# Performance work log

Measured on AMD Instinct MI355X. Metric: run time of the kernel, lower is better.

Reference implementation:

```python
import jax, jax.numpy as jnp
import numpy as np
from math import sqrt

INPUT_SIZE = 1024
HIDDEN_SIZE = 1024
OUTPUT_SIZE = 512
BATCH = 64
SEQ = 512


def _uniform(key, shape, stdv):
    return jax.random.uniform(key, shape, jnp.float32, -stdv, stdv)


def setup_inputs() -> dict:
    key = jax.random.key(0)
    ks = jax.random.split(key, 20)
    stdv = 1.0 / sqrt(HIDDEN_SIZE)
    H, I, O = HIDDEN_SIZE, INPUT_SIZE, OUTPUT_SIZE
    inp = {
        "X": jax.random.normal(ks[0], (BATCH, SEQ, I), jnp.float32),
        "c0": jnp.zeros((H, 1), jnp.float32),
        "h0": jnp.zeros((H, 1), jnp.float32),
        "w_hi": _uniform(ks[1], (H, H), stdv), "w_xi": _uniform(ks[2], (H, I), stdv),
        "b_hi": _uniform(ks[3], (H, 1), stdv), "b_xi": _uniform(ks[4], (H, 1), stdv),
        "w_hf": _uniform(ks[5], (H, H), stdv), "w_xf": _uniform(ks[6], (H, I), stdv),
        "b_hf": _uniform(ks[7], (H, 1), stdv), "b_xf": _uniform(ks[8], (H, 1), stdv),
        "w_ho": _uniform(ks[9], (H, H), stdv), "w_xo": _uniform(ks[10], (H, I), stdv),
        "b_ho": _uniform(ks[11], (H, 1), stdv), "b_xo": _uniform(ks[12], (H, 1), stdv),
        "w_hg": _uniform(ks[13], (H, H), stdv), "w_xg": _uniform(ks[14], (H, I), stdv),
        "b_hg": _uniform(ks[15], (H, 1), stdv), "b_xg": _uniform(ks[16], (H, 1), stdv),
        "w": _uniform(ks[17], (O, H), stdv),
    }
    return inp


def reference(X, c0, h0,
              w_hi, w_xi, b_hi, b_xi,
              w_hf, w_xf, b_hf, b_xf,
              w_ho, w_xo, b_ho, b_xo,
              w_hg, w_xg, b_hg, b_xg, w):
    B = X.shape[0]
    # state kept as (B, H); biases squeezed to (H,)
    bi = (b_hi + b_xi)[:, 0]
    bf = (b_hf + b_xf)[:, 0]
    bo = (b_ho + b_xo)[:, 0]
    bg = (b_hg + b_xg)[:, 0]
    h0b = jnp.broadcast_to(h0[:, 0], (B, h0.shape[0]))
    c0b = jnp.broadcast_to(c0[:, 0], (B, c0.shape[0]))

    def step(carry, x_t):  # x_t: (B, I)
        h, c = carry
        i = jax.nn.sigmoid(h @ w_hi.T + x_t @ w_xi.T + bi)
        f = jax.nn.sigmoid(h @ w_hf.T + x_t @ w_xf.T + bf)
        o = jax.nn.sigmoid(h @ w_ho.T + x_t @ w_xo.T + bo)
        g = jnp.tanh(h @ w_hg.T + x_t @ w_xg.T + bg)
        c = f * c + i * g
        h = o * jnp.tanh(c)
        return (h, c), None

    (h, c), _ = jax.lax.scan(step, (h0b, c0b), jnp.swapaxes(X, 0, 1))
    out = h @ w.T  # (B, O)
    return out[:, :, None]  # match torch output shape (B, O, 1)
```

## Files before the change

### kernel.cpp

```cpp
#include <hip/hip_runtime.h>


typedef short short8 __attribute__((ext_vector_type(8)));
typedef float f32x4 __attribute__((ext_vector_type(4)));

typedef __attribute__((address_space(1))) const unsigned int glb_u32;
typedef __attribute__((address_space(3))) unsigned int lds_u32;

#define SEQL  512
#define POISON 0xFFFFFFFFFFFFFFFFull
#define BUFU64 16384

__device__ __forceinline__ unsigned short f2bf(float f) {
    unsigned int u = __builtin_bit_cast(unsigned int, f);
    u += 0x7FFFu + ((u >> 16) & 1u);
    return (unsigned short)(u >> 16);
}
__device__ __forceinline__ float bf2f(unsigned short s) {
    unsigned int u = ((unsigned int)s) << 16;
    return __builtin_bit_cast(float, u);
}
__device__ __forceinline__ float sigmoidf_fast(float x) {
    return 1.f / (1.f + __expf(-x));
}
__device__ __forceinline__ float tanhf_fast(float x) {
    return 1.f - 2.f / (1.f + __expf(2.f * x));
}
__device__ __forceinline__ void gld_lds16(const unsigned short* g, unsigned short* l) {
    __builtin_amdgcn_global_load_lds((glb_u32*)g, (lds_u32*)l, 16, 0, 0);
}

__global__ void k_pack_w(const float* __restrict__ w0, const float* __restrict__ w1,
                         const float* __restrict__ w2, const float* __restrict__ w3,
                         unsigned short* __restrict__ dst) {
    int idx4 = blockIdx.x * blockDim.x + threadIdx.x;
    int np = idx4 >> 8;
    int k4 = (idx4 & 255) * 4;
    int g = np & 3, r = np >> 2;
    const float* src = (g == 0) ? w0 : (g == 1) ? w1 : (g == 2) ? w2 : w3;
    float4 v = *(const float4*)(src + r * 1024 + k4);
    ushort4 o;
    o.x = f2bf(v.x); o.y = f2bf(v.y); o.z = f2bf(v.z); o.w = f2bf(v.w);
    *(ushort4*)(dst + (size_t)np * 1024 + k4) = o;
}

__global__ void k_misc(const float* __restrict__ b_hi, const float* __restrict__ b_xi,
                       const float* __restrict__ b_hf, const float* __restrict__ b_xf,
                       const float* __restrict__ b_ho, const float* __restrict__ b_xo,
                       const float* __restrict__ b_hg, const float* __restrict__ b_xg,
                       const float* __restrict__ h0, const float* __restrict__ w,
                       float* __restrict__ bias, unsigned short* __restrict__ hbuf,
                       float* __restrict__ wT) {
    int idx = blockIdx.x * blockDim.x + threadIdx.x;
    if (idx < 4096) {
        int g = idx & 3, r = idx >> 2;
        const float* bh = (g == 0) ? b_hi : (g == 1) ? b_hf : (g == 2) ? b_ho : b_hg;
        const float* bx = (g == 0) ? b_xi : (g == 1) ? b_xf : (g == 2) ? b_xo : b_xg;
        bias[idx] = bh[r] + bx[r];
    } else if (idx < 4096 + 65536) {
        int e = idx - 4096;
        int k = e & 1023;
        hbuf[e] = f2bf(h0[k]);
    } else if (idx < 4096 + 65536 + 524288) {
        int e = idx - 69632;
        int k = e >> 9, o = e & 511;
        wT[e] = w[o * 1024 + k];
    } else if (idx < 4096 + 65536 + 524288 + 3 * BUFU64) {
        int e = idx - (4096 + 65536 + 524288);
        ((unsigned long long*)hbuf)[BUFU64 + e] = POISON;
    }
}

__global__ void k_convert_x(const float* __restrict__ X, unsigned short* __restrict__ Xb) {
    int idx = blockIdx.x * blockDim.x + threadIdx.x;
    float4 v = ((const float4*)X)[idx];
    ushort4 o;
    o.x = f2bf(v.x); o.y = f2bf(v.y); o.z = f2bf(v.z); o.w = f2bf(v.w);
    ((ushort4*)Xb)[idx] = o;
}

__global__ __launch_bounds__(256) void k_xgemm(const unsigned short* __restrict__ Wx,
                                               const unsigned short* __restrict__ Xb,
                                               const float* __restrict__ bias,
                                               unsigned short* __restrict__ Xg) {
    const int jt = blockIdx.x;
    const int n0 = blockIdx.y * 128;
    const int t0 = jt * 2;
    __shared__ unsigned short At[128 * 32];
    __shared__ unsigned short Bt[128 * 32];
    const int tid = threadIdx.x;
    const int w   = tid >> 6;
    const int l   = tid & 63;
    const int l15 = l & 15, lq = l >> 4;
    const int wm  = w & 1, wn = w >> 1;
    const int seg = l & 3, cr = w * 16 + (l >> 2);

    const unsigned short* gA0 = Wx + (size_t)(n0 + cr) * 1024 + seg * 8;
    const unsigned short* gA1 = gA0 + (size_t)64 * 1024;
    const unsigned short* gB0 = Xb + ((size_t)cr * 512 + t0) * 1024 + seg * 8;
    const unsigned short* gB1 = gB0 + 1024;
    unsigned short* lA0 = At + w * 512;
    unsigned short* lA1 = At + 2048 + w * 512;
    unsigned short* lB0 = Bt + w * 512;
    unsigned short* lB1 = Bt + 2048 + w * 512;

    f32x4 acc[4][4];
#pragma unroll
    for (int mi = 0; mi < 4; ++mi)
#pragma unroll
        for (int nj = 0; nj < 4; ++nj)
            acc[mi][nj] = f32x4{0.f, 0.f, 0.f, 0.f};

    for (int kk = 0; kk < 32; ++kk) {
        __syncthreads();
        gld_lds16(gA0, lA0);
        gld_lds16(gA1, lA1);
        gld_lds16(gB0, lB0);
        gld_lds16(gB1, lB1);
        gA0 += 32; gA1 += 32; gB0 += 32; gB1 += 32;
        __syncthreads();
        short8 af[4], bfr[4];
#pragma unroll
        for (int mi = 0; mi < 4; ++mi)
            af[mi] = *(const short8*)(At + (wm * 64 + mi * 16 + l15) * 32 + lq * 8);
#pragma unroll
        for (int nj = 0; nj < 4; ++nj)
            bfr[nj] = *(const short8*)(Bt + (wn * 64 + nj * 16 + l15) * 32 + lq * 8);
#pragma unroll
        for (int mi = 0; mi < 4; ++mi)
#pragma unroll
            for (int nj = 0; nj < 4; ++nj)
                acc[mi][nj] = __builtin_amdgcn_mfma_f32_16x16x32_bf16(af[mi], bfr[nj], acc[mi][nj], 0, 0, 0);
    }

#pragma unroll
    for (int mi = 0; mi < 4; ++mi) {
#pragma unroll
        for (int rr = 0; rr < 4; ++rr) {
            int np = n0 + wm * 64 + mi * 16 + lq * 4 + rr;
            float bs = bias[np];
#pragma unroll
            for (int nj = 0; nj < 4; ++nj) {
                size_t idx = ((((size_t)(t0 + wn)) * 4 + nj) * 4096 + np) * 16 + l15;
                Xg[idx] = f2bf(acc[mi][nj][rr] + bs);
            }
        }
    }
}

__global__ __launch_bounds__(512, 2) void k_rec(const unsigned short* __restrict__ Wh,
                                                const unsigned short* __restrict__ Xg,
                                                const float* __restrict__ c0,
                                                unsigned short* __restrict__ hbuf) {
    const int blk = blockIdx.x;
    const int jb  = blk & 3;
    const int ibb = blk >> 2;
    const int tid = threadIdx.x;
    const int w   = tid >> 6;
    const int l   = tid & 63;
    const int l15 = l & 15, lq = l >> 4;

    __shared__ unsigned short hTl[16 * 1032];
    __shared__ unsigned short hTr[16 * 36];

    short8 afrag[32];
    {
        const unsigned short* wrow = Wh + (size_t)(ibb * 128 + w * 16 + l15) * 1024;
#pragma unroll
        for (int ks = 0; ks < 32; ++ks)
            afrag[ks] = *(const short8*)(wrow + ks * 32 + lq * 8);
#pragma unroll
        for (int ks = 0; ks < 32; ++ks)
            asm volatile("" : "+v"(afrag[ks]));
    }

    const int hid = ibb * 32 + w * 4 + lq;
    float c = c0[hid];

    unsigned long long* hb64 = (unsigned long long*)hbuf;

    const int sb = tid >> 5, sln = tid & 31;
    const size_t prow = (size_t)(jb * 16 + sb) * 256;

    const int srow = tid >> 3, sseg = tid & 7;
    const size_t sidx = (size_t)(jb * 16 + srow) * 256 + ibb * 8 + sseg;

    const size_t xg_fix = ((size_t)ibb * 128 + w * 16 + lq * 4) * 16 + l15;

    float xg[4];
#pragma unroll
    for (int rr = 0; rr < 4; ++rr)
        xg[rr] = bf2f(Xg[((size_t)jb * 4096 + rr) * 16 + xg_fix]);

    for (int t = 0; t < SEQL; ++t) {
        {
            const unsigned long long* src = hb64 + (size_t)(t & 3) * BUFU64 + prow;
            unsigned long long tmp[8];
#pragma unroll
            for (int p = 0; p < 8; ++p)
                tmp[p] = __hip_atomic_load(src + p * 32 + sln, __ATOMIC_RELAXED,
                                           __HIP_MEMORY_SCOPE_AGENT);
            for (;;) {
                int miss = 0;
#pragma unroll
                for (int p = 0; p < 8; ++p)
                    if (tmp[p] == POISON) miss |= 1 << p;
                if (!miss) break;
                __builtin_amdgcn_s_sleep(1);
#pragma unroll
                for (int p = 0; p < 8; ++p)
                    if (miss & (1 << p))
                        tmp[p] = __hip_atomic_load(src + p * 32 + sln, __ATOMIC_RELAXED,
                                                   __HIP_MEMORY_SCOPE_AGENT);
            }
#pragma unroll
            for (int p = 0; p < 8; ++p)
                *(unsigned long long*)(&hTl[sb * 1032 + (p * 32 + sln) * 4]) = tmp[p];
        }
        __syncthreads();

        if (tid < 128)
            __hip_atomic_store(hb64 + (size_t)((t + 3) & 3) * BUFU64 + sidx, POISON,
                               __ATOMIC_RELAXED, __HIP_MEMORY_SCOPE_AGENT);

        {
            f32x4 acc0 = {0.f, 0.f, 0.f, 0.f}, acc1 = {0.f, 0.f, 0.f, 0.f};
#pragma unroll
            for (int ks = 0; ks < 32; ks += 2) {
                short8 b0 = *(const short8*)(&hTl[l15 * 1032 + ks * 32 + lq * 8]);
                short8 b1 = *(const short8*)(&hTl[l15 * 1032 + (ks + 1) * 32 + lq * 8]);
                acc0 = __builtin_amdgcn_mfma_f32_16x16x32_bf16(afrag[ks], b0, acc0, 0, 0, 0);
                acc1 = __builtin_amdgcn_mfma_f32_16x16x32_bf16(afrag[ks + 1], b1, acc1, 0, 0, 0);
            }
            float pi = acc0[0] + acc1[0] + xg[0];
            float pf = acc0[1] + acc1[1] + xg[1];
            float po = acc0[2] + acc1[2] + xg[2];
            float pg = acc0[3] + acc1[3] + xg[3];
            float ig = sigmoidf_fast(pi);
            float fg = sigmoidf_fast(pf);
            float og = sigmoidf_fast(po);
            float gg = tanhf_fast(pg);
            c = fg * c + ig * gg;
            float hh = og * tanhf_fast(c);
            hTr[l15 * 36 + w * 4 + lq] = f2bf(hh);
        }
        __syncthreads();

        if (tid < 128) {
            unsigned long long v = *(const unsigned long long*)(&hTr[srow * 36 + sseg * 4]);
            asm volatile("s_waitcnt vmcnt(0)" ::: "memory");
            __hip_atomic_store(hb64 + (size_t)((t + 1) & 3) * BUFU64 + sidx, v,
                               __ATOMIC_RELAXED, __HIP_MEMORY_SCOPE_AGENT);
        }

        if (t < SEQL - 1) {
            size_t base = (((size_t)(t + 1) * 4 + jb) * 4096) * 16 + xg_fix;
#pragma unroll
            for (int rr = 0; rr < 4; ++rr)
                xg[rr] = bf2f(Xg[base + (size_t)rr * 16]);
        }
    }
}

__global__ __launch_bounds__(256) void k_out(const unsigned short* __restrict__ hT,
                                             const float* __restrict__ wT,
                                             float* __restrict__ out) {
    const int b = blockIdx.x;
    const int tid = threadIdx.x;
    __shared__ float hs[1024];
#pragma unroll
    for (int p = 0; p < 4; ++p)
        hs[p * 256 + tid] = bf2f(hT[b * 1024 + p * 256 + tid]);
    __syncthreads();
    float a0 = 0.f, a1 = 0.f;
    for (int k = 0; k < 1024; ++k) {
        float hv = hs[k];
        a0 = fmaf(hv, wT[k * 512 + tid], a0);
        a1 = fmaf(hv, wT[k * 512 + 256 + tid], a1);
    }
    out[b * 512 + tid] = a0;
    out[b * 512 + 256 + tid] = a1;
}

extern "C" void kernel_launch(void* const* d_in, const int* in_sizes, int n_in,
                              void* d_out, int out_size, void* d_ws, size_t ws_size,
                              hipStream_t stream) {
    const float* X    = (const float*)d_in[0];
    const float* c0   = (const float*)d_in[1];
    const float* h0   = (const float*)d_in[2];
    const float* w_hi = (const float*)d_in[3];
    const float* w_xi = (const float*)d_in[4];
    const float* b_hi = (const float*)d_in[5];
    const float* b_xi = (const float*)d_in[6];
    const float* w_hf = (const float*)d_in[7];
    const float* w_xf = (const float*)d_in[8];
    const float* b_hf = (const float*)d_in[9];
    const float* b_xf = (const float*)d_in[10];
    const float* w_ho = (const float*)d_in[11];
    const float* w_xo = (const float*)d_in[12];
    const float* b_ho = (const float*)d_in[13];
    const float* b_xo = (const float*)d_in[14];
    const float* w_hg = (const float*)d_in[15];
    const float* w_xg = (const float*)d_in[16];
    const float* b_hg = (const float*)d_in[17];
    const float* b_xg = (const float*)d_in[18];
    const float* w    = (const float*)d_in[19];

    char* ws = (char*)d_ws;
    size_t off = 0;
    unsigned short* Xg  = (unsigned short*)(ws + off); off += (size_t)512 * 4096 * 64 * 2;
    unsigned short* Whp = (unsigned short*)(ws + off); off += (size_t)4096 * 1024 * 2;
    unsigned short* Wxp = (unsigned short*)(ws + off); off += (size_t)4096 * 1024 * 2;
    unsigned short* Xb  = (unsigned short*)(ws + off); off += (size_t)64 * 512 * 1024 * 2;
    float*          bias= (float*)(ws + off);          off += (size_t)4096 * 4;
    float*          wT  = (float*)(ws + off);          off += (size_t)1024 * 512 * 4;
    unsigned short* hbuf= (unsigned short*)(ws + off); off += (size_t)4 * 64 * 1024 * 2;
    if (ws_size < off) return;

    k_pack_w<<<4096, 256, 0, stream>>>(w_hi, w_hf, w_ho, w_hg, Whp);
    k_pack_w<<<4096, 256, 0, stream>>>(w_xi, w_xf, w_xo, w_xg, Wxp);
    k_misc<<<(4096 + 65536 + 524288 + 3 * BUFU64 + 255) / 256, 256, 0, stream>>>(
        b_hi, b_xi, b_hf, b_xf, b_ho, b_xo, b_hg, b_xg, h0, w, bias, hbuf, wT);
    k_convert_x<<<33554432 / 4 / 256, 256, 0, stream>>>(X, Xb);

    k_xgemm<<<dim3(256, 32), 256, 0, stream>>>(Wxp, Xb, bias, Xg);

    void* args[] = {(void*)&Whp, (void*)&Xg, (void*)&c0, (void*)&hbuf};
    hipLaunchCooperativeKernel((void*)k_rec, dim3(128), dim3(512), args, 0, stream);

    k_out<<<64, 256, 0, stream>>>(hbuf, wT, (float*)d_out);
}
```

Measured before the change: 2.053 ms.

## Replace block barriers in recurrent LSTM step with per-wave LDS flags and shuffles

The recurrent kernel no longer uses two __syncthreads per timestep. Each wave now fetches its own slice of the previous hidden state into a double-buffered LDS tile and publishes an LDS flag. Consumers spin on per-wave flags, so MFMA work on early chunks can start before every slice has arrived. The hidden-state output is packed with wave shuffles and stored directly instead of being staged in LDS, and the poison store moves to the writer side. Occupancy hint drops to one block per CU, and correctness now relies on LDS acquire/release spin-waits and the ordering of the poison writes.

```diff
diff --git a/kernel.cpp b/kernel.cpp
--- a/kernel.cpp
+++ b/kernel.cpp
@@ -148,7 +148,7 @@
     }
 }
 
-__global__ __launch_bounds__(512, 2) void k_rec(const unsigned short* __restrict__ Wh,
+__global__ __launch_bounds__(512, 1) void k_rec(const unsigned short* __restrict__ Wh,
                                                 const unsigned short* __restrict__ Xg,
                                                 const float* __restrict__ c0,
                                                 unsigned short* __restrict__ hbuf) {
@@ -160,8 +160,10 @@
     const int l   = tid & 63;
     const int l15 = l & 15, lq = l >> 4;
 
-    __shared__ unsigned short hTl[16 * 1032];
-    __shared__ unsigned short hTr[16 * 36];
+    __shared__ unsigned short hTl[2][16 * 1032];
+    __shared__ unsigned flags[2][8];
+
+    if (tid < 16) ((unsigned*)flags)[tid] = 0;
 
     short8 afrag[32];
     {
@@ -179,11 +181,11 @@
 
     unsigned long long* hb64 = (unsigned long long*)hbuf;
 
-    const int sb = tid >> 5, sln = tid & 31;
-    const size_t prow = (size_t)(jb * 16 + sb) * 256;
-
-    const int srow = tid >> 3, sseg = tid & 7;
-    const size_t sidx = (size_t)(jb * 16 + srow) * 256 + ibb * 8 + sseg;
+    const int fr = l & 15;
+    const int fseg = l >> 4;
+    const size_t rbase = (size_t)(jb * 16 + fr) * 256;
+
+    const size_t widx = (size_t)(jb * 16 + l15) * 256 + ibb * 8 + w;
 
     const size_t xg_fix = ((size_t)ibb * 128 + w * 16 + lq * 4) * 16 + l15;
 
@@ -192,46 +194,68 @@
     for (int rr = 0; rr < 4; ++rr)
         xg[rr] = bf2f(Xg[((size_t)jb * 4096 + rr) * 16 + xg_fix]);
 
+    __syncthreads();
+
     for (int t = 0; t < SEQL; ++t) {
+        const int pb = t & 1;
+
         {
-            const unsigned long long* src = hb64 + (size_t)(t & 3) * BUFU64 + prow;
+            const unsigned long long* src = hb64 + (size_t)(t & 3) * BUFU64 + rbase;
             unsigned long long tmp[8];
 #pragma unroll
-            for (int p = 0; p < 8; ++p)
-                tmp[p] = __hip_atomic_load(src + p * 32 + sln, __ATOMIC_RELAXED,
-                                           __HIP_MEMORY_SCOPE_AGENT);
+            for (int j = 0; j < 4; ++j) {
+                size_t u = (size_t)(w * 4 + j) * 8 + fseg * 2;
+                tmp[2 * j]     = __hip_atomic_load(src + u,     __ATOMIC_RELAXED,
+                                                   __HIP_MEMORY_SCOPE_AGENT);
+                tmp[2 * j + 1] = __hip_atomic_load(src + u + 1, __ATOMIC_RELAXED,
+                                                   __HIP_MEMORY_SCOPE_AGENT);
+            }
             for (;;) {
                 int miss = 0;
 #pragma unroll
-                for (int p = 0; p < 8; ++p)
-                    if (tmp[p] == POISON) miss |= 1 << p;
+                for (int j = 0; j < 8; ++j)
+                    if (tmp[j] == POISON) miss |= 1 << j;
                 if (!miss) break;
                 __builtin_amdgcn_s_sleep(1);
 #pragma unroll
-                for (int p = 0; p < 8; ++p)
-                    if (miss & (1 << p))
-                        tmp[p] = __hip_atomic_load(src + p * 32 + sln, __ATOMIC_RELAXED,
+                for (int j = 0; j < 8; ++j)
+                    if (miss & (1 << j)) {
+                        size_t u = (size_t)(w * 4 + (j >> 1)) * 8 + fseg * 2 + (j & 1);
+                        tmp[j] = __hip_atomic_load(src + u, __ATOMIC_RELAXED,
                                                    __HIP_MEMORY_SCOPE_AGENT);
-            }
-#pragma unroll
-            for (int p = 0; p < 8; ++p)
-                *(unsigned long long*)(&hTl[sb * 1032 + (p * 32 + sln) * 4]) = tmp[p];
-        }
-        __syncthreads();
-
-        if (tid < 128)
-            __hip_atomic_store(hb64 + (size_t)((t + 3) & 3) * BUFU64 + sidx, POISON,
-                               __ATOMIC_RELAXED, __HIP_MEMORY_SCOPE_AGENT);
-
+                    }
+            }
+            unsigned short* dstb = &hTl[pb][fr * 1032 + fseg * 8];
+#pragma unroll
+            for (int j = 0; j < 4; ++j) {
+                *(unsigned long long*)(dstb + (w * 4 + j) * 32)     = tmp[2 * j];
+                *(unsigned long long*)(dstb + (w * 4 + j) * 32 + 4) = tmp[2 * j + 1];
+            }
+            if (l == 0)
+                __hip_atomic_store(&flags[pb][w], (unsigned)(t + 1),
+                                   __ATOMIC_RELEASE, __HIP_MEMORY_SCOPE_WORKGROUP);
+        }
+
+        f32x4 acc0 = {0.f, 0.f, 0.f, 0.f}, acc1 = {0.f, 0.f, 0.f, 0.f};
         {
-            f32x4 acc0 = {0.f, 0.f, 0.f, 0.f}, acc1 = {0.f, 0.f, 0.f, 0.f};
-#pragma unroll
-            for (int ks = 0; ks < 32; ks += 2) {
-                short8 b0 = *(const short8*)(&hTl[l15 * 1032 + ks * 32 + lq * 8]);
-                short8 b1 = *(const short8*)(&hTl[l15 * 1032 + (ks + 1) * 32 + lq * 8]);
-                acc0 = __builtin_amdgcn_mfma_f32_16x16x32_bf16(afrag[ks], b0, acc0, 0, 0, 0);
-                acc1 = __builtin_amdgcn_mfma_f32_16x16x32_bf16(afrag[ks + 1], b1, acc1, 0, 0, 0);
-            }
+            const unsigned short* hl = &hTl[pb][0];
+#pragma unroll
+            for (int cw = 0; cw < 8; ++cw) {
+                while (__hip_atomic_load(&flags[pb][cw], __ATOMIC_ACQUIRE,
+                                         __HIP_MEMORY_SCOPE_WORKGROUP)
+                       < (unsigned)(t + 1)) { }
+#pragma unroll
+                for (int j = 0; j < 4; j += 2) {
+                    const int ks = cw * 4 + j;
+                    short8 b0 = *(const short8*)(&hl[l15 * 1032 + ks * 32 + lq * 8]);
+                    short8 b1 = *(const short8*)(&hl[l15 * 1032 + (ks + 1) * 32 + lq * 8]);
+                    acc0 = __builtin_amdgcn_mfma_f32_16x16x32_bf16(afrag[ks], b0, acc0, 0, 0, 0);
+                    acc1 = __builtin_amdgcn_mfma_f32_16x16x32_bf16(afrag[ks + 1], b1, acc1, 0, 0, 0);
+                }
+            }
+        }
+
+        {
             float pi = acc0[0] + acc1[0] + xg[0];
             float pf = acc0[1] + acc1[1] + xg[1];
             float po = acc0[2] + acc1[2] + xg[2];
@@ -242,15 +266,24 @@
             float gg = tanhf_fast(pg);
             c = fg * c + ig * gg;
             float hh = og * tanhf_fast(c);
-            hTr[l15 * 36 + w * 4 + lq] = f2bf(hh);
-        }
-        __syncthreads();
-
-        if (tid < 128) {
-            unsigned long long v = *(const unsigned long long*)(&hTr[srow * 36 + sseg * 4]);
+
+            unsigned hu = (unsigned)f2bf(hh);
+            unsigned v0 = __shfl((int)hu, l15);
+            unsigned v1 = __shfl((int)hu, l15 + 16);
+            unsigned v2 = __shfl((int)hu, l15 + 32);
+            unsigned v3 = __shfl((int)hu, l15 + 48);
+
             asm volatile("s_waitcnt vmcnt(0)" ::: "memory");
-            __hip_atomic_store(hb64 + (size_t)((t + 1) & 3) * BUFU64 + sidx, v,
-                               __ATOMIC_RELAXED, __HIP_MEMORY_SCOPE_AGENT);
+            if (l < 16) {
+                unsigned long long hv = (unsigned long long)(v0 & 0xFFFFu)
+                    | ((unsigned long long)(v1 & 0xFFFFu) << 16)
+                    | ((unsigned long long)(v2 & 0xFFFFu) << 32)
+                    | ((unsigned long long)(v3 & 0xFFFFu) << 48);
+                __hip_atomic_store(hb64 + (size_t)((t + 1) & 3) * BUFU64 + widx, hv,
+                                   __ATOMIC_RELAXED, __HIP_MEMORY_SCOPE_AGENT);
+                __hip_atomic_store(hb64 + (size_t)((t + 3) & 3) * BUFU64 + widx, POISON,
+                                   __ATOMIC_RELAXED, __HIP_MEMORY_SCOPE_AGENT);
+            }
         }
 
         if (t < SEQL - 1) {
```

Measured after the change: 4.286 ms. 109% more time.

## Fuse input projection GEMM into recurrent kernel with register-resident Wx

Applied to the files above, without the earlier changes.

Removes the separate k_xgemm kernel and its large Xg intermediate buffer. The recurrent kernel now keeps both Wh and Wx fragments in registers, streams each timestep's X slice into LDS, and computes the input projection on the fly, overlapped with the recurrence. Work is split over 256 blocks of 256 threads, each owning 16 hidden units, and the h exchange layout, the poison-reset placement and k_out indexing change to match. In exchange, register pressure roughly doubles, the per-step critical path gains the x-projection MFMAs, and the kernel uses a normal launch instead of a cooperative one while still relying on all blocks being co-resident.

```diff
diff --git a/kernel.cpp b/kernel.cpp
--- a/kernel.cpp
+++ b/kernel.cpp
@@ -59,8 +59,9 @@
         bias[idx] = bh[r] + bx[r];
     } else if (idx < 4096 + 65536) {
         int e = idx - 4096;
-        int k = e & 1023;
-        hbuf[e] = f2bf(h0[k]);
+        int cg = e >> 8;
+        int h16 = e & 15;
+        hbuf[e] = f2bf(h0[(cg & 63) * 16 + h16]);
     } else if (idx < 4096 + 65536 + 524288) {
         int e = idx - 69632;
         int k = e >> 9, o = e & 511;
@@ -79,77 +80,10 @@
     ((ushort4*)Xb)[idx] = o;
 }
 
-__global__ __launch_bounds__(256) void k_xgemm(const unsigned short* __restrict__ Wx,
-                                               const unsigned short* __restrict__ Xb,
-                                               const float* __restrict__ bias,
-                                               unsigned short* __restrict__ Xg) {
-    const int jt = blockIdx.x;
-    const int n0 = blockIdx.y * 128;
-    const int t0 = jt * 2;
-    __shared__ unsigned short At[128 * 32];
-    __shared__ unsigned short Bt[128 * 32];
-    const int tid = threadIdx.x;
-    const int w   = tid >> 6;
-    const int l   = tid & 63;
-    const int l15 = l & 15, lq = l >> 4;
-    const int wm  = w & 1, wn = w >> 1;
-    const int seg = l & 3, cr = w * 16 + (l >> 2);
-
-    const unsigned short* gA0 = Wx + (size_t)(n0 + cr) * 1024 + seg * 8;
-    const unsigned short* gA1 = gA0 + (size_t)64 * 1024;
-    const unsigned short* gB0 = Xb + ((size_t)cr * 512 + t0) * 1024 + seg * 8;
-    const unsigned short* gB1 = gB0 + 1024;
-    unsigned short* lA0 = At + w * 512;
-    unsigned short* lA1 = At + 2048 + w * 512;
-    unsigned short* lB0 = Bt + w * 512;
-    unsigned short* lB1 = Bt + 2048 + w * 512;
-
-    f32x4 acc[4][4];
-#pragma unroll
-    for (int mi = 0; mi < 4; ++mi)
-#pragma unroll
-        for (int nj = 0; nj < 4; ++nj)
-            acc[mi][nj] = f32x4{0.f, 0.f, 0.f, 0.f};
-
-    for (int kk = 0; kk < 32; ++kk) {
-        __syncthreads();
-        gld_lds16(gA0, lA0);
-        gld_lds16(gA1, lA1);
-        gld_lds16(gB0, lB0);
-        gld_lds16(gB1, lB1);
-        gA0 += 32; gA1 += 32; gB0 += 32; gB1 += 32;
-        __syncthreads();
-        short8 af[4], bfr[4];
-#pragma unroll
-        for (int mi = 0; mi < 4; ++mi)
-            af[mi] = *(const short8*)(At + (wm * 64 + mi * 16 + l15) * 32 + lq * 8);
-#pragma unroll
-        for (int nj = 0; nj < 4; ++nj)
-            bfr[nj] = *(const short8*)(Bt + (wn * 64 + nj * 16 + l15) * 32 + lq * 8);
-#pragma unroll
-        for (int mi = 0; mi < 4; ++mi)
-#pragma unroll
-            for (int nj = 0; nj < 4; ++nj)
-                acc[mi][nj] = __builtin_amdgcn_mfma_f32_16x16x32_bf16(af[mi], bfr[nj], acc[mi][nj], 0, 0, 0);
-    }
-
-#pragma unroll
-    for (int mi = 0; mi < 4; ++mi) {
-#pragma unroll
-        for (int rr = 0; rr < 4; ++rr) {
-            int np = n0 + wm * 64 + mi * 16 + lq * 4 + rr;
-            float bs = bias[np];
-#pragma unroll
-            for (int nj = 0; nj < 4; ++nj) {
-                size_t idx = ((((size_t)(t0 + wn)) * 4 + nj) * 4096 + np) * 16 + l15;
-                Xg[idx] = f2bf(acc[mi][nj][rr] + bs);
-            }
-        }
-    }
-}
-
-__global__ __launch_bounds__(512, 2) void k_rec(const unsigned short* __restrict__ Wh,
-                                                const unsigned short* __restrict__ Xg,
+__global__ __launch_bounds__(256, 1) void k_rec(const unsigned short* __restrict__ Wh,
+                                                const unsigned short* __restrict__ Wx,
+                                                const unsigned short* __restrict__ Xb,
+                                                const float* __restrict__ bias,
                                                 const float* __restrict__ c0,
                                                 unsigned short* __restrict__ hbuf) {
     const int blk = blockIdx.x;
@@ -161,103 +95,145 @@
     const int l15 = l & 15, lq = l >> 4;
 
     __shared__ unsigned short hTl[16 * 1032];
-    __shared__ unsigned short hTr[16 * 36];
-
-    short8 afrag[32];
+    __shared__ unsigned short xTl[16 * 1032];
+    __shared__ unsigned short hTr[16 * 20];
+
+    short8 afragH[32], afragX[32];
     {
-        const unsigned short* wrow = Wh + (size_t)(ibb * 128 + w * 16 + l15) * 1024;
+        const unsigned short* wrH = Wh + (size_t)(ibb * 64 + w * 16 + l15) * 1024;
+        const unsigned short* wrX = Wx + (size_t)(ibb * 64 + w * 16 + l15) * 1024;
 #pragma unroll
         for (int ks = 0; ks < 32; ++ks)
-            afrag[ks] = *(const short8*)(wrow + ks * 32 + lq * 8);
+            afragH[ks] = *(const short8*)(wrH + ks * 32 + lq * 8);
 #pragma unroll
         for (int ks = 0; ks < 32; ++ks)
-            asm volatile("" : "+v"(afrag[ks]));
-    }
-
-    const int hid = ibb * 32 + w * 4 + lq;
+            afragX[ks] = *(const short8*)(wrX + ks * 32 + lq * 8);
+#pragma unroll
+        for (int ks = 0; ks < 32; ++ks)
+            asm volatile("" : "+v"(afragH[ks]));
+    }
+
+    const int hid = ibb * 16 + w * 4 + lq;
     float c = c0[hid];
+    float bias4[4];
+#pragma unroll
+    for (int rr = 0; rr < 4; ++rr)
+        bias4[rr] = bias[(size_t)ibb * 64 + w * 16 + lq * 4 + rr];
 
     unsigned long long* hb64 = (unsigned long long*)hbuf;
 
-    const int sb = tid >> 5, sln = tid & 31;
-    const size_t prow = (size_t)(jb * 16 + sb) * 256;
-
-    const int srow = tid >> 3, sseg = tid & 7;
-    const size_t sidx = (size_t)(jb * 16 + srow) * 256 + ibb * 8 + sseg;
-
-    const size_t xg_fix = ((size_t)ibb * 128 + w * 16 + lq * 4) * 16 + l15;
+    const int sbb = (tid >> 2) & 15, sl4 = tid & 3;
+    const int stage_sh = sbb * 1032 + w * 16 + sl4 * 4;
+
+#pragma unroll
+    for (int i = 0; i < 8; ++i) {
+        int r = w * 8 + i, b16 = r >> 1, half = r & 1;
+        const unsigned short* src =
+            Xb + ((size_t)(jb * 16 + b16) * 512 + 0) * 1024 + half * 512 + l * 8;
+        gld_lds16(src, &xTl[b16 * 1032 + half * 512]);
+    }
+    asm volatile("s_waitcnt vmcnt(0)" ::: "memory");
+    __syncthreads();
 
     float xg[4];
-#pragma unroll
-    for (int rr = 0; rr < 4; ++rr)
-        xg[rr] = bf2f(Xg[((size_t)jb * 4096 + rr) * 16 + xg_fix]);
+    {
+        f32x4 xa0 = {0.f, 0.f, 0.f, 0.f}, xa1 = {0.f, 0.f, 0.f, 0.f};
+#pragma unroll
+        for (int ks = 0; ks < 32; ks += 2) {
+            short8 b0 = *(const short8*)(&xTl[l15 * 1032 + ks * 32 + lq * 8]);
+            short8 b1 = *(const short8*)(&xTl[l15 * 1032 + (ks + 1) * 32 + lq * 8]);
+            xa0 = __builtin_amdgcn_mfma_f32_16x16x32_bf16(afragX[ks], b0, xa0, 0, 0, 0);
+            xa1 = __builtin_amdgcn_mfma_f32_16x16x32_bf16(afragX[ks + 1], b1, xa1, 0, 0, 0);
+        }
+#pragma unroll
+        for (int rr = 0; rr < 4; ++rr)
+            xg[rr] = xa0[rr] + xa1[rr] + bias4[rr];
+    }
 
     for (int t = 0; t < SEQL; ++t) {
         {
-            const unsigned long long* src = hb64 + (size_t)(t & 3) * BUFU64 + prow;
-            unsigned long long tmp[8];
-#pragma unroll
-            for (int p = 0; p < 8; ++p)
-                tmp[p] = __hip_atomic_load(src + p * 32 + sln, __ATOMIC_RELAXED,
+            const unsigned long long* src =
+                hb64 + (size_t)(t & 3) * BUFU64 + (size_t)jb * 4096 + tid;
+            unsigned long long tmp[16];
+#pragma unroll
+            for (int p = 0; p < 16; ++p)
+                tmp[p] = __hip_atomic_load(src + p * 256, __ATOMIC_RELAXED,
                                            __HIP_MEMORY_SCOPE_AGENT);
             for (;;) {
-                int miss = 0;
-#pragma unroll
-                for (int p = 0; p < 8; ++p)
-                    if (tmp[p] == POISON) miss |= 1 << p;
+                unsigned miss = 0;
+#pragma unroll
+                for (int p = 0; p < 16; ++p)
+                    if (tmp[p] == POISON) miss |= 1u << p;
                 if (!miss) break;
                 __builtin_amdgcn_s_sleep(1);
 #pragma unroll
-                for (int p = 0; p < 8; ++p)
-                    if (miss & (1 << p))
-                        tmp[p] = __hip_atomic_load(src + p * 32 + sln, __ATOMIC_RELAXED,
+                for (int p = 0; p < 16; ++p)
+                    if (miss & (1u << p))
+                        tmp[p] = __hip_atomic_load(src + p * 256, __ATOMIC_RELAXED,
                                                    __HIP_MEMORY_SCOPE_AGENT);
             }
 #pragma unroll
-            for (int p = 0; p < 8; ++p)
-                *(unsigned long long*)(&hTl[sb * 1032 + (p * 32 + sln) * 4]) = tmp[p];
+            for (int p = 0; p < 16; ++p)
+                *(unsigned long long*)(&hTl[stage_sh + p * 64]) = tmp[p];
         }
         __syncthreads();
 
-        if (tid < 128)
-            __hip_atomic_store(hb64 + (size_t)((t + 3) & 3) * BUFU64 + sidx, POISON,
-                               __ATOMIC_RELAXED, __HIP_MEMORY_SCOPE_AGENT);
+        if (t < SEQL - 1) {
+#pragma unroll
+            for (int i = 0; i < 8; ++i) {
+                int r = w * 8 + i, b16 = r >> 1, half = r & 1;
+                const unsigned short* src =
+                    Xb + ((size_t)(jb * 16 + b16) * 512 + (t + 1)) * 1024 + half * 512 + l * 8;
+                gld_lds16(src, &xTl[b16 * 1032 + half * 512]);
+            }
+        }
 
         {
-            f32x4 acc0 = {0.f, 0.f, 0.f, 0.f}, acc1 = {0.f, 0.f, 0.f, 0.f};
+            f32x4 a0 = {0.f, 0.f, 0.f, 0.f}, a1 = {0.f, 0.f, 0.f, 0.f};
 #pragma unroll
             for (int ks = 0; ks < 32; ks += 2) {
                 short8 b0 = *(const short8*)(&hTl[l15 * 1032 + ks * 32 + lq * 8]);
                 short8 b1 = *(const short8*)(&hTl[l15 * 1032 + (ks + 1) * 32 + lq * 8]);
-                acc0 = __builtin_amdgcn_mfma_f32_16x16x32_bf16(afrag[ks], b0, acc0, 0, 0, 0);
-                acc1 = __builtin_amdgcn_mfma_f32_16x16x32_bf16(afrag[ks + 1], b1, acc1, 0, 0, 0);
+                a0 = __builtin_amdgcn_mfma_f32_16x16x32_bf16(afragH[ks], b0, a0, 0, 0, 0);
+                a1 = __builtin_amdgcn_mfma_f32_16x16x32_bf16(afragH[ks + 1], b1, a1, 0, 0, 0);
             }
-            float pi = acc0[0] + acc1[0] + xg[0];
-            float pf = acc0[1] + acc1[1] + xg[1];
-            float po = acc0[2] + acc1[2] + xg[2];
-            float pg = acc0[3] + acc1[3] + xg[3];
+            float pi = a0[0] + a1[0] + xg[0];
+            float pf = a0[1] + a1[1] + xg[1];
+            float po = a0[2] + a1[2] + xg[2];
+            float pg = a0[3] + a1[3] + xg[3];
             float ig = sigmoidf_fast(pi);
             float fg = sigmoidf_fast(pf);
             float og = sigmoidf_fast(po);
             float gg = tanhf_fast(pg);
             c = fg * c + ig * gg;
             float hh = og * tanhf_fast(c);
-            hTr[l15 * 36 + w * 4 + lq] = f2bf(hh);
+            hTr[l15 * 20 + w * 4 + lq] = f2bf(hh);
         }
         __syncthreads();
 
-        if (tid < 128) {
-            unsigned long long v = *(const unsigned long long*)(&hTr[srow * 36 + sseg * 4]);
+        if (tid < 64) {
+            int b = tid >> 2, l4 = tid & 3;
+            unsigned long long v = *(const unsigned long long*)(&hTr[b * 20 + l4 * 4]);
             asm volatile("s_waitcnt vmcnt(0)" ::: "memory");
-            __hip_atomic_store(hb64 + (size_t)((t + 1) & 3) * BUFU64 + sidx, v,
+            size_t u = (size_t)(jb * 64 + ibb) * 64 + b * 4 + l4;
+            __hip_atomic_store(hb64 + (size_t)((t + 1) & 3) * BUFU64 + u, v,
                                __ATOMIC_RELAXED, __HIP_MEMORY_SCOPE_AGENT);
+            __hip_atomic_store(hb64 + (size_t)((t + 3) & 3) * BUFU64 + u, POISON,
+                               __ATOMIC_RELAXED, __HIP_MEMORY_SCOPE_AGENT);
         }
 
         if (t < SEQL - 1) {
-            size_t base = (((size_t)(t + 1) * 4 + jb) * 4096) * 16 + xg_fix;
+            f32x4 xa0 = {0.f, 0.f, 0.f, 0.f}, xa1 = {0.f, 0.f, 0.f, 0.f};
+#pragma unroll
+            for (int ks = 0; ks < 32; ks += 2) {
+                short8 b0 = *(const short8*)(&xTl[l15 * 1032 + ks * 32 + lq * 8]);
+                short8 b1 = *(const short8*)(&xTl[l15 * 1032 + (ks + 1) * 32 + lq * 8]);
+                xa0 = __builtin_amdgcn_mfma_f32_16x16x32_bf16(afragX[ks], b0, xa0, 0, 0, 0);
+                xa1 = __builtin_amdgcn_mfma_f32_16x16x32_bf16(afragX[ks + 1], b1, xa1, 0, 0, 0);
+            }
 #pragma unroll
             for (int rr = 0; rr < 4; ++rr)
-                xg[rr] = bf2f(Xg[base + (size_t)rr * 16]);
+                xg[rr] = xa0[rr] + xa1[rr] + bias4[rr];
         }
     }
 }
@@ -266,11 +242,14 @@
                                              const float* __restrict__ wT,
                                              float* __restrict__ out) {
     const int b = blockIdx.x;
+    const int jb = b >> 4, b16 = b & 15;
     const int tid = threadIdx.x;
     __shared__ float hs[1024];
 #pragma unroll
-    for (int p = 0; p < 4; ++p)
-        hs[p * 256 + tid] = bf2f(hT[b * 1024 + p * 256 + tid]);
+    for (int p = 0; p < 4; ++p) {
+        int k = p * 256 + tid;
+        hs[k] = bf2f(hT[(size_t)(jb * 64 + (k >> 4)) * 256 + b16 * 16 + (k & 15)]);
+    }
     __syncthreads();
     float a0 = 0.f, a1 = 0.f;
     for (int k = 0; k < 1024; ++k) {
@@ -308,7 +287,6 @@
 
     char* ws = (char*)d_ws;
     size_t off = 0;
-    unsigned short* Xg  = (unsigned short*)(ws + off); off += (size_t)512 * 4096 * 64 * 2;
     unsigned short* Whp = (unsigned short*)(ws + off); off += (size_t)4096 * 1024 * 2;
     unsigned short* Wxp = (unsigned short*)(ws + off); off += (size_t)4096 * 1024 * 2;
     unsigned short* Xb  = (unsigned short*)(ws + off); off += (size_t)64 * 512 * 1024 * 2;
@@ -323,10 +301,7 @@
         b_hi, b_xi, b_hf, b_xf, b_ho, b_xo, b_hg, b_xg, h0, w, bias, hbuf, wT);
     k_convert_x<<<33554432 / 4 / 256, 256, 0, stream>>>(X, Xb);
 
-    k_xgemm<<<dim3(256, 32), 256, 0, stream>>>(Wxp, Xb, bias, Xg);
-
-    void* args[] = {(void*)&Whp, (void*)&Xg, (void*)&c0, (void*)&hbuf};
-    hipLaunchCooperativeKernel((void*)k_rec, dim3(128), dim3(512), args, 0, stream);
+    k_rec<<<dim3(256), dim3(256), 0, stream>>>(Whp, Wxp, Xb, bias, c0, hbuf);
 
     k_out<<<64, 256, 0, stream>>>(hbuf, wT, (float*)d_out);
 }
```

After: 1.820 ms. -11.4%, faster.
